# Performance work log

Hardware: AMD Instinct MI355X
Metric: run time of the kernel (lower is better)

## Reference

```python
import jax, jax.numpy as jnp
import numpy as np

B, H, S, D = 2, 16, 2048, 64


def setup_inputs() -> dict:
    key = jax.random.key(0)
    kq, kk, kv = jax.random.split(key, 3)
    queries = jax.random.normal(kq, (B, H, S, D), dtype=jnp.float32)
    keys = jax.random.normal(kk, (B, H, S, D), dtype=jnp.float32)
    values = jax.random.normal(kv, (B, H, S, D), dtype=jnp.float32)
    scaling_factor = jnp.asarray(np.sqrt(D), dtype=jnp.float32)
    # causal mask, broadcast over heads: True = attend
    causal = jnp.tril(jnp.ones((S, S), dtype=bool))
    mask = jnp.broadcast_to(causal[None, None, :, :], (B, 1, S, S))
    return {
        "queries": queries,
        "keys": keys,
        "values": values,
        "scaling_factor": scaling_factor,
        "mask": mask,
    }


def reference(queries, keys, values, scaling_factor, mask):
    # scores: [B, H, S, S]
    scores = jnp.einsum("bhqd,bhkd->bhqk", queries, keys) / scaling_factor
    scores = jnp.where(mask, scores, -jnp.inf)
    attn = jax.nn.softmax(scores, axis=-1)
    # embeddings: [B, H, S, D]
    return jnp.einsum("bhqk,bhkd->bhqd", attn, values)
```

## Files before the change

### kernel.cpp

```cpp
#include <hip/hip_runtime.h>
#include <hip/hip_bf16.h>


typedef __attribute__((ext_vector_type(8))) short bf16x8;
typedef __attribute__((ext_vector_type(4))) float f32x4;
typedef unsigned uint2v __attribute__((ext_vector_type(2)));

#define MFMA32K(a, b, c) __builtin_amdgcn_mfma_f32_16x16x32_bf16(a, b, c, 0, 0, 0)

constexpr int Bsz = 2, Hn = 16, Sn = 2048, Dn = 64;
constexpr int QBLK = 64, KBLK = 64;
constexpr int NE = Bsz * Hn * Sn * Dn;

#if defined(__has_builtin)
#if __has_builtin(__builtin_amdgcn_exp2f)
#define EXP2(x) __builtin_amdgcn_exp2f(x)
#endif
#endif
#ifndef EXP2
#define EXP2(x) exp2f(x)
#endif

__device__ inline short f2bf(float f) {
  union { float f; unsigned u; } v;
  v.f = f;
  unsigned r = v.u + 0x7FFF + ((v.u >> 16) & 1);
  return (short)(r >> 16);
}

__device__ inline unsigned pk_bf16(float lo, float hi) {
  unsigned r;
  asm("v_cvt_pk_bf16_f32 %0, %1, %2" : "=v"(r) : "v"(lo), "v"(hi));
  return r;
}

__device__ inline void gl2lds16(const void* g, void* l) {
  __builtin_amdgcn_global_load_lds(
      (const __attribute__((address_space(1))) unsigned int*)g,
      (__attribute__((address_space(3))) unsigned int*)l, 16, 0, 0);
}

__device__ inline int swz(int row, int colbyte) {
  return row * 128 + (colbyte ^ ((row & 7) << 4));
}

#if defined(__has_builtin)
#if __has_builtin(__builtin_amdgcn_permlane16_swap) && \
    __has_builtin(__builtin_amdgcn_permlane32_swap)
#define HAVE_PERMLANE_SWAP 1
#endif
#endif

__device__ inline float xred_max(float x) {
#ifdef HAVE_PERMLANE_SWAP
  uint2v a = __builtin_amdgcn_permlane16_swap(__float_as_uint(x),
                                              __float_as_uint(x), false, false);
  x = fmaxf(__uint_as_float(a[0]), __uint_as_float(a[1]));
  uint2v b = __builtin_amdgcn_permlane32_swap(__float_as_uint(x),
                                              __float_as_uint(x), false, false);
  x = fmaxf(__uint_as_float(b[0]), __uint_as_float(b[1]));
#else
  x = fmaxf(x, __shfl_xor(x, 16, 64));
  x = fmaxf(x, __shfl_xor(x, 32, 64));
#endif
  return x;
}

__global__ __launch_bounds__(256) void prep(const float* __restrict__ K,
                                            const float* __restrict__ V,
                                            short* __restrict__ Kb,
                                            short* __restrict__ Vt) {
  const int tile = blockIdx.x, bh = blockIdx.y;
  const int tid = threadIdx.x;
  const int r = tid >> 2, c = (tid & 3) * 16;
  const size_t base = (size_t)bh * Sn * Dn;

  if (blockIdx.z == 0) {
    const float* kp = K + base + (size_t)(tile * 64 + r) * Dn + c;
    float4 x0 = *(const float4*)(kp + 0);
    float4 x1 = *(const float4*)(kp + 4);
    float4 x2 = *(const float4*)(kp + 8);
    float4 x3 = *(const float4*)(kp + 12);
    bf16x8 w0, w1;
    w0[0] = f2bf(x0.x); w0[1] = f2bf(x0.y); w0[2] = f2bf(x0.z); w0[3] = f2bf(x0.w);
    w0[4] = f2bf(x1.x); w0[5] = f2bf(x1.y); w0[6] = f2bf(x1.z); w0[7] = f2bf(x1.w);
    w1[0] = f2bf(x2.x); w1[1] = f2bf(x2.y); w1[2] = f2bf(x2.z); w1[3] = f2bf(x2.w);
    w1[4] = f2bf(x3.x); w1[5] = f2bf(x3.y); w1[6] = f2bf(x3.z); w1[7] = f2bf(x3.w);
    short* op = Kb + base + (size_t)(tile * 64 + r) * Dn + c;
    *(bf16x8*)op = w0;
    *(bf16x8*)(op + 8) = w1;
  } else {
    __shared__ short t[64][66];
    const float* vp = V + base + (size_t)(tile * 64 + r) * Dn + c;
    float4 x0 = *(const float4*)(vp + 0);
    float4 x1 = *(const float4*)(vp + 4);
    float4 x2 = *(const float4*)(vp + 8);
    float4 x3 = *(const float4*)(vp + 12);
    short* tr = &t[r][c];
    tr[0] = f2bf(x0.x); tr[1] = f2bf(x0.y); tr[2] = f2bf(x0.z); tr[3] = f2bf(x0.w);
    tr[4] = f2bf(x1.x); tr[5] = f2bf(x1.y); tr[6] = f2bf(x1.z); tr[7] = f2bf(x1.w);
    tr[8] = f2bf(x2.x); tr[9] = f2bf(x2.y); tr[10] = f2bf(x2.z); tr[11] = f2bf(x2.w);
    tr[12] = f2bf(x3.x); tr[13] = f2bf(x3.y); tr[14] = f2bf(x3.z); tr[15] = f2bf(x3.w);
    __syncthreads();
    short* op = Vt + base + (size_t)r * Sn + tile * 64 + c;
    bf16x8 w0, w1;
#pragma unroll
    for (int j = 0; j < 8; ++j) {
      int p0 = c + j, p1 = c + 8 + j;
      int k0 = 32 * (p0 >> 5) + 16 * ((p0 >> 2) & 1) + 4 * ((p0 >> 3) & 3) + (p0 & 3);
      int k1 = 32 * (p1 >> 5) + 16 * ((p1 >> 2) & 1) + 4 * ((p1 >> 3) & 3) + (p1 & 3);
      w0[j] = t[k0][r];
      w1[j] = t[k1][r];
    }
    *(bf16x8*)op = w0;
    *(bf16x8*)(op + 8) = w1;
  }
}

__global__ __launch_bounds__(256, 4) void attn_fwd(
    const float* __restrict__ Q, const short* __restrict__ Kb,
    const short* __restrict__ Vt, const float* __restrict__ SF,
    float* __restrict__ O) {
  __shared__ short Kbuf[2][64 * 64];
  __shared__ short Vbuf[2][64 * 64];

  const int bh = blockIdx.x;
  const int qt = (gridDim.y - 1) - blockIdx.y;
  const int tid = threadIdx.x;
  const int wave = tid >> 6, lane = tid & 63;
  const int g = lane >> 4, lc = lane & 15;
  const float qscale = 1.4426950408889634f / SF[0];

  const size_t base = (size_t)bh * Sn * Dn;
  const int qg = qt * QBLK + wave * 16 + lc;

  int ka[4][2], va[2][4];
#pragma unroll
  for (int t = 0; t < 4; ++t) {
    ka[t][0] = swz(t * 16 + lc, g * 16);
    ka[t][1] = swz(t * 16 + lc, g * 16 + 64);
  }
#pragma unroll
  for (int t2 = 0; t2 < 2; ++t2)
#pragma unroll
    for (int dt = 0; dt < 4; ++dt)
      va[t2][dt] = swz(dt * 16 + lc, t2 * 64 + g * 16);
  int koff[2], voff[2];
#pragma unroll
  for (int j = 0; j < 2; ++j) {
    int c = wave * 2 + j;
    int off = c * 1024 + lane * 16;
    int row = off >> 7;
    int col = (off & 127) ^ ((row & 7) << 4);
    koff[j] = row * 128 + col;
    voff[j] = row * (Sn * 2) + col;
  }

  const char* kpg = (const char*)(Kb + base);
  const char* vpg = (const char*)(Vt + base);

  auto stageK = [&](int buf) {
#pragma unroll
    for (int j = 0; j < 2; ++j)
      gl2lds16(kpg + koff[j], (char*)Kbuf[buf] + (wave * 2 + j) * 1024);
    kpg += KBLK * Dn * 2;
  };
  auto stageV = [&](int buf) {
#pragma unroll
    for (int j = 0; j < 2; ++j)
      gl2lds16(vpg + voff[j], (char*)Vbuf[buf] + (wave * 2 + j) * 1024);
    vpg += KBLK * 2;
  };

  bf16x8 bq[2];
  {
    const float* qp = Q + base + (size_t)qg * Dn + g * 8;
#pragma unroll
    for (int h = 0; h < 2; ++h) {
      float4 x0 = *(const float4*)(qp + 32 * h);
      float4 x1 = *(const float4*)(qp + 32 * h + 4);
      bf16x8 a;
      a[0] = f2bf(x0.x * qscale); a[1] = f2bf(x0.y * qscale);
      a[2] = f2bf(x0.z * qscale); a[3] = f2bf(x0.w * qscale);
      a[4] = f2bf(x1.x * qscale); a[5] = f2bf(x1.y * qscale);
      a[6] = f2bf(x1.z * qscale); a[7] = f2bf(x1.w * qscale);
      bq[h] = a;
    }
  }

  bf16x8 ones;
#pragma unroll
  for (int j = 0; j < 8; ++j) ones[j] = (short)0x3F80;

  f32x4 o[4], lsum = (f32x4){0.f, 0.f, 0.f, 0.f};
#pragma unroll
  for (int dt = 0; dt < 4; ++dt) o[dt] = (f32x4){0.f, 0.f, 0.f, 0.f};
  float m = -10000.0f;

  int cur = 0;
  stageK(0);
  stageV(0);
  __syncthreads();

  auto tile_body = [&](int cur_, bool stage_next, bool masked, int kb) {
    const char* Kc = (const char*)Kbuf[cur_];
    const char* Vc = (const char*)Vbuf[cur_];

    f32x4 s[4];
    __builtin_amdgcn_s_setprio(1);
#pragma unroll
    for (int t = 0; t < 4; ++t) {
      bf16x8 ak0 = *(const bf16x8*)(Kc + ka[t][0]);
      bf16x8 ak1 = *(const bf16x8*)(Kc + ka[t][1]);
      f32x4 z = (f32x4){0.f, 0.f, 0.f, 0.f};
      z = MFMA32K(ak0, bq[0], z);
      z = MFMA32K(ak1, bq[1], z);
      s[t] = z;
    }
    __builtin_amdgcn_s_setprio(0);

    if (masked) {
#pragma unroll
      for (int t = 0; t < 4; ++t)
#pragma unroll
        for (int i = 0; i < 4; ++i) {
          int kg = kb + t * 16 + g * 4 + i;
          if (kg > qg) s[t][i] = -30000.0f;
        }
    }

    float a0 = fmaxf(fmaxf(s[0][0], s[0][1]), s[0][2]);
    float a1 = fmaxf(fmaxf(s[0][3], s[1][0]), s[1][1]);
    float a2 = fmaxf(fmaxf(s[1][2], s[1][3]), s[2][0]);
    float a3 = fmaxf(fmaxf(s[2][1], s[2][2]), s[2][3]);
    float a4 = fmaxf(fmaxf(s[3][0], s[3][1]), s[3][2]);
    float b0 = fmaxf(fmaxf(a0, a1), a2);
    float b1 = fmaxf(fmaxf(a3, a4), s[3][3]);
    float plocal = fmaxf(b0, b1);
    if (!__all(plocal - m <= 8.0f)) {
      float pmax = xred_max(plocal);
      float mnew = fmaxf(m, pmax);
      float alpha = EXP2(m - mnew);
      lsum[0] *= alpha;
#pragma unroll
      for (int dt = 0; dt < 4; ++dt) o[dt] *= alpha;
      m = mnew;
    }
#pragma unroll
    for (int t = 0; t < 4; ++t)
#pragma unroll
      for (int i = 0; i < 4; ++i) s[t][i] = EXP2(s[t][i] - m);

    union { unsigned uu[4]; bf16x8 v; } pb[2];
#pragma unroll
    for (int t2 = 0; t2 < 2; ++t2) {
      pb[t2].uu[0] = pk_bf16(s[2 * t2][0], s[2 * t2][1]);
      pb[t2].uu[1] = pk_bf16(s[2 * t2][2], s[2 * t2][3]);
      pb[t2].uu[2] = pk_bf16(s[2 * t2 + 1][0], s[2 * t2 + 1][1]);
      pb[t2].uu[3] = pk_bf16(s[2 * t2 + 1][2], s[2 * t2 + 1][3]);
    }
    __builtin_amdgcn_s_setprio(1);
#pragma unroll
    for (int t2 = 0; t2 < 2; ++t2) {
      lsum = MFMA32K(ones, pb[t2].v, lsum);
#pragma unroll
      for (int dt = 0; dt < 4; ++dt) {
        bf16x8 av = *(const bf16x8*)(Vc + va[t2][dt]);
        o[dt] = MFMA32K(av, pb[t2].v, o[dt]);
      }
    }
    __builtin_amdgcn_s_setprio(0);

    __syncthreads();
  };

  for (int kt = 0; kt < qt; ++kt) {
    stageK(cur ^ 1);
    stageV(cur ^ 1);
    tile_body(cur, true, false, 0);
    cur ^= 1;
  }
  tile_body(cur, false, true, qt * KBLK);

  const float inv = 1.0f / lsum[0];
  float* op = O + base + (size_t)qg * Dn;
#pragma unroll
  for (int dt = 0; dt < 4; ++dt) {
    f32x4 r = o[dt] * inv;
    *(f32x4*)(op + dt * 16 + g * 4) = r;
  }
}

extern "C" void kernel_launch(void* const* d_in, const int* in_sizes, int n_in,
                              void* d_out, int out_size, void* d_ws, size_t ws_size,
                              hipStream_t stream) {
  const float* Q = (const float*)d_in[0];
  const float* K = (const float*)d_in[1];
  const float* V = (const float*)d_in[2];
  const float* SF = (const float*)d_in[3];
  float* O = (float*)d_out;

  short* Kb = (short*)d_ws;
  short* Vt = Kb + NE;

  prep<<<dim3(Sn / 64, Bsz * Hn, 2), 256, 0, stream>>>(K, V, Kb, Vt);
  attn_fwd<<<dim3(Bsz * Hn, Sn / QBLK), 256, 0, stream>>>(Q, Kb, Vt, SF, O);
}
```

Measured before the change: 48.77 us.

## Halve query block, stream V from global into registers, stage only K

Shrinks the query block from 64 to 32 rows and runs 128-thread blocks, doubling the grid so the causal triangle is split more finely across CUs. V fragments are now read straight from global memory into registers at the start of each tile instead of being staged through shared memory, and only K is double-buffered in LDS. The last tile skips the barrier. In exchange, each wave fetches V redundantly from cache and K reuse per block is halved, while register pressure rises from holding the V fragments.

```diff
diff --git a/kernel.cpp b/kernel.cpp
--- a/kernel.cpp
+++ b/kernel.cpp
@@ -9,7 +9,7 @@
 #define MFMA32K(a, b, c) __builtin_amdgcn_mfma_f32_16x16x32_bf16(a, b, c, 0, 0, 0)
 
 constexpr int Bsz = 2, Hn = 16, Sn = 2048, Dn = 64;
-constexpr int QBLK = 64, KBLK = 64;
+constexpr int QBLK = 32, KBLK = 64;
 constexpr int NE = Bsz * Hn * Sn * Dn;
 
 #if defined(__has_builtin)
@@ -117,60 +117,49 @@
   }
 }
 
-__global__ __launch_bounds__(256, 4) void attn_fwd(
+__global__ __launch_bounds__(128) void attn_fwd(
     const float* __restrict__ Q, const short* __restrict__ Kb,
     const short* __restrict__ Vt, const float* __restrict__ SF,
     float* __restrict__ O) {
   __shared__ short Kbuf[2][64 * 64];
-  __shared__ short Vbuf[2][64 * 64];
 
   const int bh = blockIdx.x;
-  const int qt = (gridDim.y - 1) - blockIdx.y;
+  const int qtq = (gridDim.y - 1) - blockIdx.y;
   const int tid = threadIdx.x;
   const int wave = tid >> 6, lane = tid & 63;
   const int g = lane >> 4, lc = lane & 15;
   const float qscale = 1.4426950408889634f / SF[0];
 
   const size_t base = (size_t)bh * Sn * Dn;
-  const int qg = qt * QBLK + wave * 16 + lc;
-
-  int ka[4][2], va[2][4];
+  const int qg = qtq * QBLK + wave * 16 + lc;
+  const int nkv = (qtq >> 1) + 1;
+
+  int ka[4][2];
 #pragma unroll
   for (int t = 0; t < 4; ++t) {
     ka[t][0] = swz(t * 16 + lc, g * 16);
     ka[t][1] = swz(t * 16 + lc, g * 16 + 64);
   }
-#pragma unroll
-  for (int t2 = 0; t2 < 2; ++t2)
-#pragma unroll
-    for (int dt = 0; dt < 4; ++dt)
-      va[t2][dt] = swz(dt * 16 + lc, t2 * 64 + g * 16);
-  int koff[2], voff[2];
-#pragma unroll
-  for (int j = 0; j < 2; ++j) {
-    int c = wave * 2 + j;
-    int off = c * 1024 + lane * 16;
+  int koff[4];
+#pragma unroll
+  for (int j = 0; j < 4; ++j) {
+    int off = (wave * 4 + j) * 1024 + lane * 16;
     int row = off >> 7;
-    int col = (off & 127) ^ ((row & 7) << 4);
-    koff[j] = row * 128 + col;
-    voff[j] = row * (Sn * 2) + col;
+    koff[j] = row * 128 + ((off & 127) ^ ((row & 7) << 4));
   }
 
   const char* kpg = (const char*)(Kb + base);
-  const char* vpg = (const char*)(Vt + base);
-
   auto stageK = [&](int buf) {
 #pragma unroll
-    for (int j = 0; j < 2; ++j)
-      gl2lds16(kpg + koff[j], (char*)Kbuf[buf] + (wave * 2 + j) * 1024);
+    for (int j = 0; j < 4; ++j)
+      gl2lds16(kpg + koff[j], (char*)Kbuf[buf] + (wave * 4 + j) * 1024);
     kpg += KBLK * Dn * 2;
   };
-  auto stageV = [&](int buf) {
-#pragma unroll
-    for (int j = 0; j < 2; ++j)
-      gl2lds16(vpg + voff[j], (char*)Vbuf[buf] + (wave * 2 + j) * 1024);
-    vpg += KBLK * 2;
-  };
+
+  const char* vb[4];
+#pragma unroll
+  for (int dt = 0; dt < 4; ++dt)
+    vb[dt] = (const char*)(Vt + base) + (size_t)(dt * 16 + lc) * (Sn * 2) + g * 16;
 
   bf16x8 bq[2];
   {
@@ -199,12 +188,19 @@
 
   int cur = 0;
   stageK(0);
-  stageV(0);
   __syncthreads();
 
-  auto tile_body = [&](int cur_, bool stage_next, bool masked, int kb) {
+  auto tile_body = [&](int cur_, int kt, bool do_stage, bool masked, int kb) {
+    bf16x8 vf[2][4];
+#pragma unroll
+    for (int t2 = 0; t2 < 2; ++t2)
+#pragma unroll
+      for (int dt = 0; dt < 4; ++dt)
+        vf[t2][dt] = *(const bf16x8*)(vb[dt] + kt * 128 + t2 * 64);
+
+    if (do_stage) stageK(cur_ ^ 1);
+
     const char* Kc = (const char*)Kbuf[cur_];
-    const char* Vc = (const char*)Vbuf[cur_];
 
     f32x4 s[4];
     __builtin_amdgcn_s_setprio(1);
@@ -264,23 +260,19 @@
     for (int t2 = 0; t2 < 2; ++t2) {
       lsum = MFMA32K(ones, pb[t2].v, lsum);
 #pragma unroll
-      for (int dt = 0; dt < 4; ++dt) {
-        bf16x8 av = *(const bf16x8*)(Vc + va[t2][dt]);
-        o[dt] = MFMA32K(av, pb[t2].v, o[dt]);
-      }
+      for (int dt = 0; dt < 4; ++dt)
+        o[dt] = MFMA32K(vf[t2][dt], pb[t2].v, o[dt]);
     }
     __builtin_amdgcn_s_setprio(0);
 
-    __syncthreads();
+    if (do_stage) __syncthreads();
   };
 
-  for (int kt = 0; kt < qt; ++kt) {
-    stageK(cur ^ 1);
-    stageV(cur ^ 1);
-    tile_body(cur, true, false, 0);
+  for (int kt = 0; kt < nkv - 1; ++kt) {
+    tile_body(cur, kt, true, false, 0);
     cur ^= 1;
   }
-  tile_body(cur, false, true, qt * KBLK);
+  tile_body(cur, nkv - 1, false, true, (nkv - 1) * KBLK);
 
   const float inv = 1.0f / lsum[0];
   float* op = O + base + (size_t)qg * Dn;
@@ -304,5 +296,5 @@
   short* Vt = Kb + NE;
 
   prep<<<dim3(Sn / 64, Bsz * Hn, 2), 256, 0, stream>>>(K, V, Kb, Vt);
-  attn_fwd<<<dim3(Bsz * Hn, Sn / QBLK), 256, 0, stream>>>(Q, Kb, Vt, SF, O);
-}
+  attn_fwd<<<dim3(Bsz * Hn, Sn / QBLK), 128, 0, stream>>>(Q, Kb, Vt, SF, O);
+}
```

Result: slower. 88.57 us (+81.6%).
